# Kernel optimization log

Measured on AMD Instinct MI355X. Metric: run time of the kernel, lower is better.

Reference implementation:

```python
import jax, jax.numpy as jnp
import numpy as np

B, S, E, H = 2, 2048, 1024, 16
D = E // H  # head size = 64


def setup_inputs() -> dict:
    key = jax.random.key(0)
    ks = jax.random.split(key, 13)
    scale = 1.0 / np.sqrt(E)
    inp = {
        "q": jax.random.normal(ks[0], (B, S, E), jnp.float32),
        "k": jax.random.normal(ks[1], (B, S, E), jnp.float32),
        "v": jax.random.normal(ks[2], (B, S, E), jnp.float32),
        "mask": jax.random.randint(ks[3], (B, 1, S, S), 0, 2, jnp.int32),
        "Wq": jax.random.normal(ks[4], (E, E), jnp.float32) * scale,
        "bq": jnp.zeros((E,), jnp.float32),
        "Wk": jax.random.normal(ks[5], (E, E), jnp.float32) * scale,
        "bk": jnp.zeros((E,), jnp.float32),
        "Wv": jax.random.normal(ks[6], (E, E), jnp.float32) * scale,
        "bv": jnp.zeros((E,), jnp.float32),
        "Wo": jax.random.normal(ks[7], (E, E), jnp.float32) * scale,
        "bo": jnp.zeros((E,), jnp.float32),
    }
    return inp


def reference(q, k, v, mask, Wq, bq, Wk, bk, Wv, bv, Wo, bo):
    # Linear projections (torch Linear: x @ W.T + b)
    qh = (q @ Wq.T + bq).reshape(B, S, H, D).transpose(0, 2, 1, 3)  # [B,H,S,D]
    kh = (k @ Wk.T + bk).reshape(B, S, H, D).transpose(0, 2, 1, 3)
    vh = (v @ Wv.T + bv).reshape(B, S, H, D).transpose(0, 2, 1, 3)

    scores = jnp.einsum("bhqd,bhkd->bhqk", qh, kh) / jnp.sqrt(jnp.float32(D))
    scores = jnp.where(mask == 0, jnp.float32(-1e10), scores)
    attn = jax.nn.softmax(scores, axis=-1)  # [B,H,S,S]
    ctx = jnp.einsum("bhqk,bhkd->bhqd", attn, vh)  # dropout p=0.0 -> identity

    out = ctx.transpose(0, 2, 1, 3).reshape(B, S, E)
    return out @ Wo.T + bo
```

## Files before the change

kernel.cpp:

```cpp
#include <hip/hip_runtime.h>

typedef unsigned short ushort_t;
typedef __attribute__((ext_vector_type(8))) short short8;
typedef __attribute__((ext_vector_type(4))) float f32x4;
typedef __attribute__((ext_vector_type(4))) unsigned short ushort4_t;
typedef __attribute__((ext_vector_type(2))) unsigned int uint2_t;
typedef __attribute__((ext_vector_type(4))) unsigned int uint4_t;

#define BB 2
#define SS 2048
#define EE 1024
#define HH 16
#define DD 64
#define MM (BB*SS)

#define QB_OFF  0u
#define KB_OFF  4194304u
#define VB_OFF  8388608u
#define WQ_OFF  12582912u
#define WK_OFF  13631488u
#define WV_OFF  14680064u
#define WO_OFF  15728640u
#define QH_OFF  16777216u
#define KH_OFF  20971520u
#define VT_OFF  25165824u
#define CTX_OFF QB_OFF
#define MB_OFF  29360128u

__device__ __forceinline__ ushort_t f2bf(float x) {
    unsigned u = __builtin_bit_cast(unsigned, x);
    u += 0x7FFFu + ((u >> 16) & 1u);
    return (ushort_t)(u >> 16);
}

__device__ __forceinline__ unsigned pk_bf16(float a, float b) {
    unsigned ua = __builtin_bit_cast(unsigned, a);
    unsigned ub = __builtin_bit_cast(unsigned, b);
    ua += 0x7FFFu + ((ua >> 16) & 1u);
    ub += 0x7FFFu + ((ub >> 16) & 1u);
    return __builtin_amdgcn_perm(ub, ua, 0x07060302u);
}

__device__ __forceinline__ void load_lds16(const void* g, void* l) {
    __builtin_amdgcn_global_load_lds((const __attribute__((address_space(1))) void*)g,
                                     (__attribute__((address_space(3))) void*)l, 16, 0, 0);
}

__global__ __launch_bounds__(256) void prep_kernel(
    const float* __restrict__ q, const float* __restrict__ k, const float* __restrict__ v,
    const int* __restrict__ mask,
    const float* __restrict__ Wq, const float* __restrict__ Wk,
    const float* __restrict__ Wv, const float* __restrict__ Wo,
    ushort_t* __restrict__ wsb, unsigned* __restrict__ maskbits)
{
    int g = blockIdx.x;
    if (g < 16384) {
        int idx = g * 256 + threadIdx.x;
        const float* src; ushort_t* dst; int rel;
        if      (idx < 1048576) { src = q;  dst = wsb + QB_OFF; rel = idx; }
        else if (idx < 2097152) { src = k;  dst = wsb + KB_OFF; rel = idx - 1048576; }
        else if (idx < 3145728) { src = v;  dst = wsb + VB_OFF; rel = idx - 2097152; }
        else if (idx < 3407872) { src = Wq; dst = wsb + WQ_OFF; rel = idx - 3145728; }
        else if (idx < 3670016) { src = Wk; dst = wsb + WK_OFF; rel = idx - 3407872; }
        else if (idx < 3932160) { src = Wv; dst = wsb + WV_OFF; rel = idx - 3670016; }
        else                    { src = Wo; dst = wsb + WO_OFF; rel = idx - 3932160; }
        f32x4 val = ((const f32x4*)src)[rel];
        ushort4_t o;
        o.x = f2bf(val.x); o.y = f2bf(val.y); o.z = f2bf(val.z); o.w = f2bf(val.w);
        ((ushort4_t*)dst)[rel] = o;
    } else {
        int t = (g - 16384) * 256 + threadIdx.x;
        int b   = t >> 17;
        int rem = t & 131071;
        int w   = rem >> 11;
        int sk  = rem & 2047;
        unsigned bits = 0;
        const int* mp = mask + ((size_t)b * SS + (size_t)w * 32) * SS + sk;
        #pragma unroll
        for (int jj = 0; jj < 32; ++jj)
            bits |= (mp[(size_t)jj * SS] != 0 ? 1u : 0u) << jj;
        maskbits[((size_t)b * SS + sk) * 64 + w] = bits;
    }
}

__device__ __forceinline__ void gemm_mainloop(
    const ushort_t* __restrict__ A, const ushort_t* __restrict__ Bm,
    int m0, int n0, f32x4 acc[4][4], ushort_t* As, ushort_t* Bs)
{
    const int tid  = threadIdx.x;
    const int wave = tid >> 6, lane = tid & 63;
    const int r16  = lane >> 2;
    const int c8   = (lane & 3) * 8;
    const int lane15 = lane & 15, quad = lane >> 4;
    const int wm = wave >> 1, wn = wave & 1;

    #pragma unroll 1
    for (int kt = 0; kt < 16; ++kt) {
        const int k0 = kt * 64;
        __syncthreads();
        #pragma unroll
        for (int s = 0; s < 2; ++s) {
            const ushort_t* ga = A  + (size_t)(m0 + wave * 32 + r16) * 1024 + k0 + s * 32 + c8;
            load_lds16(ga,             As + s * 4096 + wave * 1024);
            load_lds16(ga + 16 * 1024, As + s * 4096 + wave * 1024 + 512);
            const ushort_t* gb = Bm + (size_t)(n0 + wave * 32 + r16) * 1024 + k0 + s * 32 + c8;
            load_lds16(gb,             Bs + s * 4096 + wave * 1024);
            load_lds16(gb + 16 * 1024, Bs + s * 4096 + wave * 1024 + 512);
        }
        __syncthreads();

        #pragma unroll
        for (int s = 0; s < 2; ++s) {
            short8 a[4], bf[4];
            #pragma unroll
            for (int i = 0; i < 4; ++i)
                a[i] = *(const short8*)&As[s * 4096 + (wm * 64 + i * 16 + lane15) * 32 + quad * 8];
            #pragma unroll
            for (int j = 0; j < 4; ++j)
                bf[j] = *(const short8*)&Bs[s * 4096 + (wn * 64 + j * 16 + lane15) * 32 + quad * 8];
            #pragma unroll
            for (int i = 0; i < 4; ++i)
                #pragma unroll
                for (int j = 0; j < 4; ++j)
                    acc[i][j] = __builtin_amdgcn_mfma_f32_16x16x32_bf16(a[i], bf[j], acc[i][j], 0, 0, 0);
        }
    }
}

__global__ __launch_bounds__(256) void gemm_qkv(
    ushort_t* __restrict__ wsb,
    const float* __restrict__ bq, const float* __restrict__ bk, const float* __restrict__ bv)
{
    __shared__ ushort_t As[2 * 4096], Bs[2 * 4096];
    const int z = blockIdx.z;
    const ushort_t* A;
    const ushort_t* Bm;
    if      (z == 0) { A = wsb + QB_OFF; Bm = wsb + WQ_OFF; }
    else if (z == 1) { A = wsb + KB_OFF; Bm = wsb + WK_OFF; }
    else             { A = wsb + WV_OFF; Bm = wsb + VB_OFF; }
    const float* bias  = (z == 0) ? bq : (z == 1) ? bk : bv;
    ushort_t* dst      = wsb + (z == 0 ? QH_OFF : z == 1 ? KH_OFF : VT_OFF);
    const int m0 = (z < 2) ? blockIdx.y * 128 : blockIdx.x * 128;
    const int n0 = (z < 2) ? blockIdx.x * 128 : blockIdx.y * 128;

    f32x4 acc[4][4];
    #pragma unroll
    for (int i = 0; i < 4; ++i)
        #pragma unroll
        for (int j = 0; j < 4; ++j) acc[i][j] = (f32x4){0.f, 0.f, 0.f, 0.f};

    gemm_mainloop(A, Bm, m0, n0, acc, As, Bs);

    const int tid = threadIdx.x, wave = tid >> 6, lane = tid & 63;
    const int lane15 = lane & 15, quad = lane >> 4;
    const int wm = wave >> 1, wn = wave & 1;
    const float scale = (z == 0) ? 0.180336880111f : 1.0f;

    if (z < 2) {
        #pragma unroll
        for (int i = 0; i < 4; ++i) {
            #pragma unroll
            for (int j = 0; j < 4; ++j) {
                int col = n0 + wn * 64 + j * 16 + lane15;
                float bv_ = bias[col];
                int hh = col >> 6, d = col & 63;
                #pragma unroll
                for (int r = 0; r < 4; ++r) {
                    int row = m0 + wm * 64 + i * 16 + quad * 4 + r;
                    int bb = row >> 11, s = row & 2047;
                    float val = (acc[i][j][r] + bv_) * scale;
                    dst[(((size_t)bb * HH + hh) * SS + s) * DD + d] = f2bf(val);
                }
            }
        }
    } else {
        #pragma unroll
        for (int i = 0; i < 4; ++i) {
            #pragma unroll
            for (int r = 0; r < 4; ++r) {
                int row = m0 + wm * 64 + i * 16 + quad * 4 + r;
                float bv_ = bias[row];
                int hh = row >> 6, d = row & 63;
                #pragma unroll
                for (int j = 0; j < 4; ++j) {
                    int col = n0 + wn * 64 + j * 16 + lane15;
                    int bb = col >> 11, s = col & 2047;
                    int kk = s & 127;
                    int sp = ((kk >> 6) << 6) | ((kk & 15) << 2) | ((kk >> 4) & 3);
                    dst[(((size_t)bb * HH + hh) * DD + d) * SS + (s & ~127) + sp]
                        = f2bf(acc[i][j][r] + bv_);
                }
            }
        }
    }
}

__global__ __launch_bounds__(256, 2) void attn_kernel(
    const ushort_t* __restrict__ wsb, const unsigned* __restrict__ maskbits,
    ushort_t* __restrict__ ctx)
{
    __shared__ ushort_t Ks[128 * 64];
    __shared__ ushort_t Vts[64 * 128];
    __shared__ ushort_t Ps[128 * 64];

    const int tid  = threadIdx.x;
    const int wave = tid >> 6, lane = tid & 63;
    const int lane15 = lane & 15, quad = lane >> 4;
    const int sw7 = lane15 & 7;
    const int bh = blockIdx.y;
    const int b  = bh >> 4, h = bh & 15;
    const int q0 = blockIdx.x * 128;

    const ushort_t* Qh  = wsb + QH_OFF;
    const ushort_t* Kh  = wsb + KH_OFF;
    const ushort_t* VhT = wsb + VT_OFF;

    short8 qfrag[2][2];
    #pragma unroll
    for (int i = 0; i < 2; ++i)
        #pragma unroll
        for (int ks = 0; ks < 2; ++ks)
            qfrag[i][ks] = *(const short8*)(Qh +
                ((size_t)bh * SS + q0 + wave * 32 + i * 16 + lane15) * DD + ks * 32 + quad * 8);

    short8 ones_frag;
    {
        short onev = (lane15 == 0) ? (short)0x3F80 : (short)0;
        #pragma unroll
        for (int e = 0; e < 8; ++e) ones_frag[e] = onev;
    }

    const f32x4 zero4 = (f32x4){0.f, 0.f, 0.f, 0.f};
    f32x4 s_acc[2][8];
    f32x4 o_acc[2][4];
    f32x4 osum[2];
    #pragma unroll
    for (int i = 0; i < 2; ++i) {
        #pragma unroll
        for (int jd = 0; jd < 4; ++jd) o_acc[i][jd] = zero4;
        osum[i] = zero4;
    }

    #pragma unroll 1
    for (int kt = 0; kt < 16; ++kt) {
        const int k0 = kt * 128;
        __syncthreads();

        const ushort_t* Kbase = Kh + ((size_t)bh * SS + k0) * DD;
        #pragma unroll
        for (int cc = 0; cc < 4; ++cc) {
            int n = (wave * 4 + cc) * 64 + lane;
            int row = n >> 3;
            int c = (n & 7) ^ (row & 7);
            load_lds16(Kbase + row * 64 + c * 8, Ks + (wave * 4 + cc) * 512);
        }
        const ushort_t* Vbase = VhT + ((size_t)bh * DD) * SS + k0;
        #pragma unroll
        for (int cc = 0; cc < 4; ++cc) {
            int n = (wave * 4 + cc) * 64 + lane;
            int d = n >> 4;
            int c = (n & 15) ^ (d & 7);
            load_lds16(Vbase + (size_t)d * SS + c * 8, Vts + (wave * 4 + cc) * 512);
        }

        unsigned mw[8];
        {
            const int qw = (q0 >> 5) + wave;
            #pragma unroll
            for (int j = 0; j < 8; ++j) {
                int sk = k0 + j * 16 + lane15;
                mw[j] = maskbits[((size_t)b * SS + sk) * 64 + qw];
            }
        }
        __syncthreads();

        #pragma unroll
        for (int j = 0; j < 8; ++j) {
            short8 bf = *(const short8*)&Ks[(j * 16 + lane15) * 64 + ((quad ^ sw7) << 3)];
            s_acc[0][j] = __builtin_amdgcn_mfma_f32_16x16x32_bf16(qfrag[0][0], bf, zero4, 0, 0, 0);
            s_acc[1][j] = __builtin_amdgcn_mfma_f32_16x16x32_bf16(qfrag[1][0], bf, zero4, 0, 0, 0);
        }
        #pragma unroll
        for (int j = 0; j < 8; ++j) {
            short8 bf = *(const short8*)&Ks[(j * 16 + lane15) * 64 + (((4 + quad) ^ sw7) << 3)];
            s_acc[0][j] = __builtin_amdgcn_mfma_f32_16x16x32_bf16(qfrag[0][1], bf, s_acc[0][j], 0, 0, 0);
            s_acc[1][j] = __builtin_amdgcn_mfma_f32_16x16x32_bf16(qfrag[1][1], bf, s_acc[1][j], 0, 0, 0);
        }

        #pragma unroll
        for (int ph = 0; ph < 2; ++ph) {
            #pragma unroll
            for (int i = 0; i < 2; ++i) {
                #pragma unroll
                for (int r = 0; r < 4; ++r) {
                    const int bit = i * 16 + quad * 4 + r;
                    float p[4];
                    #pragma unroll
                    for (int jj = 0; jj < 4; ++jj) {
                        float e = __builtin_amdgcn_exp2f(s_acc[i][ph * 4 + jj][r]);
                        p[jj] = ((mw[ph * 4 + jj] >> bit) & 1u) ? e : 0.f;
                    }
                    uint2_t pk;
                    pk.x = pk_bf16(p[0], p[1]);
                    pk.y = pk_bf16(p[2], p[3]);
                    const int row = wave * 32 + i * 16 + quad * 4 + r;
                    *(uint2_t*)&Ps[row * 64 +
                        ((((lane15 >> 1) ^ (row & 7)) << 3) + ((lane15 & 1) << 2))] = pk;
                }
            }

            #pragma unroll
            for (int kb = 0; kb < 2; ++kb) {
                short8 ap[2];
                #pragma unroll
                for (int i = 0; i < 2; ++i)
                    ap[i] = *(const short8*)&Ps[(wave * 32 + i * 16 + lane15) * 64 +
                                                (((kb * 4 + quad) ^ sw7) << 3)];
                #pragma unroll
                for (int jd = 0; jd < 4; ++jd) {
                    short8 bv_ = *(const short8*)&Vts[(jd * 16 + lane15) * 128 +
                                                      (((ph * 8 + kb * 4 + quad) ^ sw7) << 3)];
                    o_acc[0][jd] = __builtin_amdgcn_mfma_f32_16x16x32_bf16(ap[0], bv_, o_acc[0][jd], 0, 0, 0);
                    o_acc[1][jd] = __builtin_amdgcn_mfma_f32_16x16x32_bf16(ap[1], bv_, o_acc[1][jd], 0, 0, 0);
                }
                osum[0] = __builtin_amdgcn_mfma_f32_16x16x32_bf16(ap[0], ones_frag, osum[0], 0, 0, 0);
                osum[1] = __builtin_amdgcn_mfma_f32_16x16x32_bf16(ap[1], ones_frag, osum[1], 0, 0, 0);
            }
        }
    }

    #pragma unroll
    for (int i = 0; i < 2; ++i) {
        #pragma unroll
        for (int r = 0; r < 4; ++r) {
            float l = __shfl(osum[i][r], lane & 48);
            float inv = 1.0f / l;
            int row = q0 + wave * 32 + i * 16 + quad * 4 + r;
            #pragma unroll
            for (int jd = 0; jd < 4; ++jd) {
                int col = h * DD + jd * 16 + lane15;
                ctx[((size_t)b * SS + row) * EE + col] = f2bf(o_acc[i][jd][r] * inv);
            }
        }
    }
}

__global__ __launch_bounds__(256) void gemm_out(
    const ushort_t* __restrict__ wsb, const float* __restrict__ bo, float* __restrict__ out)
{
    __shared__ ushort_t As[2 * 2048];
    __shared__ ushort_t Bs[2 * 4096];
    const ushort_t* A  = wsb + CTX_OFF;
    const ushort_t* Bm = wsb + WO_OFF;
    const int m0 = blockIdx.y * 64, n0 = blockIdx.x * 128;

    const int tid = threadIdx.x, wave = tid >> 6, lane = tid & 63;
    const int lane15 = lane & 15, quad = lane >> 4;

    f32x4 acc[8];
    #pragma unroll
    for (int j = 0; j < 8; ++j) acc[j] = (f32x4){0.f, 0.f, 0.f, 0.f};

    #pragma unroll 1
    for (int kt = 0; kt < 16; ++kt) {
        const int k0 = kt * 64;
        __syncthreads();
        #pragma unroll
        for (int s = 0; s < 2; ++s) {
            {
                int n = wave * 64 + lane;
                load_lds16(A + (size_t)(m0 + (n >> 2)) * 1024 + k0 + s * 32 + (n & 3) * 8,
                           As + s * 2048 + wave * 512);
            }
            #pragma unroll
            for (int m = 0; m < 2; ++m) {
                int n = m * 256 + wave * 64 + lane;
                load_lds16(Bm + (size_t)(n0 + (n >> 2)) * 1024 + k0 + s * 32 + (n & 3) * 8,
                           Bs + s * 4096 + (m * 256 + wave * 64) * 8);
            }
        }
        __syncthreads();

        #pragma unroll
        for (int s = 0; s < 2; ++s) {
            short8 a = *(const short8*)&As[s * 2048 + (wave * 16 + lane15) * 32 + quad * 8];
            #pragma unroll
            for (int j = 0; j < 8; ++j) {
                short8 bf = *(const short8*)&Bs[s * 4096 + (j * 16 + lane15) * 32 + quad * 8];
                acc[j] = __builtin_amdgcn_mfma_f32_16x16x32_bf16(a, bf, acc[j], 0, 0, 0);
            }
        }
    }

    #pragma unroll
    for (int j = 0; j < 8; ++j) {
        int col = n0 + j * 16 + lane15;
        float bv_ = bo[col];
        #pragma unroll
        for (int r = 0; r < 4; ++r) {
            int row = m0 + wave * 16 + quad * 4 + r;
            out[(size_t)row * EE + col] = acc[j][r] + bv_;
        }
    }
}

extern "C" void kernel_launch(void* const* d_in, const int* in_sizes, int n_in,
                              void* d_out, int out_size, void* d_ws, size_t ws_size,
                              hipStream_t stream) {
    const float* q    = (const float*)d_in[0];
    const float* k    = (const float*)d_in[1];
    const float* v    = (const float*)d_in[2];
    const int*   mask = (const int*)  d_in[3];
    const float* Wq   = (const float*)d_in[4];
    const float* bq   = (const float*)d_in[5];
    const float* Wk   = (const float*)d_in[6];
    const float* bk   = (const float*)d_in[7];
    const float* Wv   = (const float*)d_in[8];
    const float* bv   = (const float*)d_in[9];
    const float* Wo   = (const float*)d_in[10];
    const float* bo   = (const float*)d_in[11];

    ushort_t* wsb = (ushort_t*)d_ws;
    unsigned* maskbits = (unsigned*)(wsb + MB_OFF);

    prep_kernel<<<17408, 256, 0, stream>>>(q, k, v, mask, Wq, Wk, Wv, Wo, wsb, maskbits);
    gemm_qkv<<<dim3(8, 32, 3), 256, 0, stream>>>(wsb, bq, bk, bv);
    attn_kernel<<<dim3(16, 32), 256, 0, stream>>>(wsb, maskbits, wsb + CTX_OFF);
    gemm_out<<<dim3(8, 64), 256, 0, stream>>>(wsb, bo, (float*)d_out);
}
```

Baseline: 283.2 us.

## Keep attention probabilities in registers via transposed S MFMA, drop P LDS staging

Computes S transposed (K fragment as A operand) so each lane's exp'd scores directly form the A-operand fragment of the PV MFMA, eliminating the Ps shared-memory write/read round trip. The V-transpose permutation in the projection epilogue and the mask bitpacking layout (now row-major per query using wave ballots) are changed to match the new register layout. This removes LDS traffic and a buffer, at the cost of tighter coupling between the permutation, mask layout and MFMA lane mapping.

```diff
diff --git a/kernel.cpp b/kernel.cpp
--- a/kernel.cpp
+++ b/kernel.cpp
@@ -4,7 +4,6 @@
 typedef __attribute__((ext_vector_type(8))) short short8;
 typedef __attribute__((ext_vector_type(4))) float f32x4;
 typedef __attribute__((ext_vector_type(4))) unsigned short ushort4_t;
-typedef __attribute__((ext_vector_type(2))) unsigned int uint2_t;
 typedef __attribute__((ext_vector_type(4))) unsigned int uint4_t;
 
 #define BB 2
@@ -69,17 +68,19 @@
         o.x = f2bf(val.x); o.y = f2bf(val.y); o.z = f2bf(val.z); o.w = f2bf(val.w);
         ((ushort4_t*)dst)[rel] = o;
     } else {
-        int t = (g - 16384) * 256 + threadIdx.x;
-        int b   = t >> 17;
-        int rem = t & 131071;
-        int w   = rem >> 11;
-        int sk  = rem & 2047;
-        unsigned bits = 0;
-        const int* mp = mask + ((size_t)b * SS + (size_t)w * 32) * SS + sk;
-        #pragma unroll
-        for (int jj = 0; jj < 32; ++jj)
-            bits |= (mp[(size_t)jj * SS] != 0 ? 1u : 0u) << jj;
-        maskbits[((size_t)b * SS + sk) * 64 + w] = bits;
+        const int lane = threadIdx.x & 63;
+        int wid = (g - 16384) * 4 + (threadIdx.x >> 6);
+        int b = wid >> 11, qr = wid & 2047;
+        const int* mp = mask + ((size_t)b * SS + qr) * SS;
+        unsigned* outw = maskbits + ((size_t)b * SS + qr) * 64;
+        #pragma unroll 4
+        for (int k0 = 0; k0 < SS; k0 += 64) {
+            unsigned long long bal = __ballot(mp[k0 + lane] != 0);
+            if (lane == 0) {
+                outw[(k0 >> 5)]     = (unsigned)bal;
+                outw[(k0 >> 5) + 1] = (unsigned)(bal >> 32);
+            }
+        }
     }
 }
 
@@ -186,7 +187,7 @@
                     int col = n0 + wn * 64 + j * 16 + lane15;
                     int bb = col >> 11, s = col & 2047;
                     int kk = s & 127;
-                    int sp = ((kk >> 6) << 6) | ((kk & 15) << 2) | ((kk >> 4) & 3);
+                    int sp = (kk & 0x60) | ((kk & 12) << 1) | ((kk & 16) >> 2) | (kk & 3);
                     dst[(((size_t)bb * HH + hh) * DD + d) * SS + (s & ~127) + sp]
                         = f2bf(acc[i][j][r] + bv_);
                 }
@@ -201,7 +202,6 @@
 {
     __shared__ ushort_t Ks[128 * 64];
     __shared__ ushort_t Vts[64 * 128];
-    __shared__ ushort_t Ps[128 * 64];
 
     const int tid  = threadIdx.x;
     const int wave = tid >> 6, lane = tid & 63;
@@ -263,69 +263,62 @@
             load_lds16(Vbase + (size_t)d * SS + c * 8, Vts + (wave * 4 + cc) * 512);
         }
 
-        unsigned mw[8];
+        unsigned mw2[2][4];
         {
-            const int qw = (q0 >> 5) + wave;
-            #pragma unroll
-            for (int j = 0; j < 8; ++j) {
-                int sk = k0 + j * 16 + lane15;
-                mw[j] = maskbits[((size_t)b * SS + sk) * 64 + qw];
+            const int kw0 = k0 >> 5;
+            #pragma unroll
+            for (int i = 0; i < 2; ++i) {
+                const size_t qrow = (size_t)b * SS + q0 + wave * 32 + i * 16 + lane15;
+                #pragma unroll
+                for (int w = 0; w < 4; ++w)
+                    mw2[i][w] = maskbits[qrow * 64 + kw0 + w];
             }
         }
         __syncthreads();
 
         #pragma unroll
         for (int j = 0; j < 8; ++j) {
-            short8 bf = *(const short8*)&Ks[(j * 16 + lane15) * 64 + ((quad ^ sw7) << 3)];
-            s_acc[0][j] = __builtin_amdgcn_mfma_f32_16x16x32_bf16(qfrag[0][0], bf, zero4, 0, 0, 0);
-            s_acc[1][j] = __builtin_amdgcn_mfma_f32_16x16x32_bf16(qfrag[1][0], bf, zero4, 0, 0, 0);
+            short8 kf = *(const short8*)&Ks[(j * 16 + lane15) * 64 + ((quad ^ sw7) << 3)];
+            s_acc[0][j] = __builtin_amdgcn_mfma_f32_16x16x32_bf16(kf, qfrag[0][0], zero4, 0, 0, 0);
+            s_acc[1][j] = __builtin_amdgcn_mfma_f32_16x16x32_bf16(kf, qfrag[1][0], zero4, 0, 0, 0);
         }
         #pragma unroll
         for (int j = 0; j < 8; ++j) {
-            short8 bf = *(const short8*)&Ks[(j * 16 + lane15) * 64 + (((4 + quad) ^ sw7) << 3)];
-            s_acc[0][j] = __builtin_amdgcn_mfma_f32_16x16x32_bf16(qfrag[0][1], bf, s_acc[0][j], 0, 0, 0);
-            s_acc[1][j] = __builtin_amdgcn_mfma_f32_16x16x32_bf16(qfrag[1][1], bf, s_acc[1][j], 0, 0, 0);
-        }
-
-        #pragma unroll
-        for (int ph = 0; ph < 2; ++ph) {
+            short8 kf = *(const short8*)&Ks[(j * 16 + lane15) * 64 + (((4 + quad) ^ sw7) << 3)];
+            s_acc[0][j] = __builtin_amdgcn_mfma_f32_16x16x32_bf16(kf, qfrag[0][1], s_acc[0][j], 0, 0, 0);
+            s_acc[1][j] = __builtin_amdgcn_mfma_f32_16x16x32_bf16(kf, qfrag[1][1], s_acc[1][j], 0, 0, 0);
+        }
+
+        #pragma unroll
+        for (int ks = 0; ks < 4; ++ks) {
+            short8 ap[2];
             #pragma unroll
             for (int i = 0; i < 2; ++i) {
+                float p[2][4];
                 #pragma unroll
-                for (int r = 0; r < 4; ++r) {
-                    const int bit = i * 16 + quad * 4 + r;
-                    float p[4];
+                for (int hf = 0; hf < 2; ++hf) {
                     #pragma unroll
-                    for (int jj = 0; jj < 4; ++jj) {
-                        float e = __builtin_amdgcn_exp2f(s_acc[i][ph * 4 + jj][r]);
-                        p[jj] = ((mw[ph * 4 + jj] >> bit) & 1u) ? e : 0.f;
+                    for (int r = 0; r < 4; ++r) {
+                        float e = __builtin_amdgcn_exp2f(s_acc[i][ks * 2 + hf][r]);
+                        p[hf][r] = ((mw2[i][ks] >> (hf * 16 + quad * 4 + r)) & 1u) ? e : 0.f;
                     }
-                    uint2_t pk;
-                    pk.x = pk_bf16(p[0], p[1]);
-                    pk.y = pk_bf16(p[2], p[3]);
-                    const int row = wave * 32 + i * 16 + quad * 4 + r;
-                    *(uint2_t*)&Ps[row * 64 +
-                        ((((lane15 >> 1) ^ (row & 7)) << 3) + ((lane15 & 1) << 2))] = pk;
                 }
-            }
-
-            #pragma unroll
-            for (int kb = 0; kb < 2; ++kb) {
-                short8 ap[2];
-                #pragma unroll
-                for (int i = 0; i < 2; ++i)
-                    ap[i] = *(const short8*)&Ps[(wave * 32 + i * 16 + lane15) * 64 +
-                                                (((kb * 4 + quad) ^ sw7) << 3)];
-                #pragma unroll
-                for (int jd = 0; jd < 4; ++jd) {
-                    short8 bv_ = *(const short8*)&Vts[(jd * 16 + lane15) * 128 +
-                                                      (((ph * 8 + kb * 4 + quad) ^ sw7) << 3)];
-                    o_acc[0][jd] = __builtin_amdgcn_mfma_f32_16x16x32_bf16(ap[0], bv_, o_acc[0][jd], 0, 0, 0);
-                    o_acc[1][jd] = __builtin_amdgcn_mfma_f32_16x16x32_bf16(ap[1], bv_, o_acc[1][jd], 0, 0, 0);
-                }
-                osum[0] = __builtin_amdgcn_mfma_f32_16x16x32_bf16(ap[0], ones_frag, osum[0], 0, 0, 0);
-                osum[1] = __builtin_amdgcn_mfma_f32_16x16x32_bf16(ap[1], ones_frag, osum[1], 0, 0, 0);
-            }
+                uint4_t api;
+                api.x = pk_bf16(p[0][0], p[0][1]);
+                api.y = pk_bf16(p[0][2], p[0][3]);
+                api.z = pk_bf16(p[1][0], p[1][1]);
+                api.w = pk_bf16(p[1][2], p[1][3]);
+                ap[i] = __builtin_bit_cast(short8, api);
+            }
+            #pragma unroll
+            for (int jd = 0; jd < 4; ++jd) {
+                short8 bv_ = *(const short8*)&Vts[(jd * 16 + lane15) * 128 +
+                                                  (((ks * 4 + quad) ^ sw7) << 3)];
+                o_acc[0][jd] = __builtin_amdgcn_mfma_f32_16x16x32_bf16(ap[0], bv_, o_acc[0][jd], 0, 0, 0);
+                o_acc[1][jd] = __builtin_amdgcn_mfma_f32_16x16x32_bf16(ap[1], bv_, o_acc[1][jd], 0, 0, 0);
+            }
+            osum[0] = __builtin_amdgcn_mfma_f32_16x16x32_bf16(ap[0], ones_frag, osum[0], 0, 0, 0);
+            osum[1] = __builtin_amdgcn_mfma_f32_16x16x32_bf16(ap[1], ones_frag, osum[1], 0, 0, 0);
         }
     }
 
```

New measurement: 282.7 us. No clear change (-0.2%).
